# Kernel optimization log

Hardware: AMD Instinct MI355X
Metric: run time of the kernel (lower is better)

## Reference

```python
import jax, jax.numpy as jnp
import numpy as np

WH, WW = 8, 8            # window_size
SH = 2                   # shuffle
NH = 6                   # num_heads
ED = 96                  # embed_dim
NP = WH * WW             # num_patches = 64
S2 = SH * SH             # shuffle group = 4
HD = ED // NH            # head_dim = 16
SCALE = HD ** -0.5 / SH
NW = 2048
NWM = 64
EPS = 1e-5


def _rel_pos_index():
    coords = np.stack(np.meshgrid(np.arange(WH), np.arange(WW), indexing='ij'))  # (2, wh, ww)
    cf = coords.reshape(2, -1)                                # (2, np)
    rel = (cf[:, :, None] - cf[:, None, :]).transpose(1, 2, 0).astype(np.int64)  # (np, np, 2)
    rel[..., 0] += WH - 1
    rel[..., 1] += WW - 1
    rel[..., 0] *= 2 * WW - 1
    return rel.sum(-1).reshape(-1)                            # (np*np,)

_REL_IDX = jnp.asarray(_rel_pos_index())


def setup_inputs() -> dict:
    key = jax.random.key(0)
    ks = jax.random.split(key, 6)
    return {
        'query': jax.random.normal(ks[0], (NW, NP * S2, ED), dtype=jnp.float32),
        'key': jax.random.normal(ks[1], (NW, NP * S2, ED), dtype=jnp.float32),
        'value': jax.random.normal(ks[2], (NW, NP * S2, ED), dtype=jnp.float32),
        'mask': jax.random.normal(ks[3], (NWM, NP, NP), dtype=jnp.float32),
        'bias_table': jax.random.normal(ks[4], (( 2 * WH - 1) * (2 * WW - 1), NH), dtype=jnp.float32) * 0.02,
        'norm_gamma': jnp.ones((S2, ED), dtype=jnp.float32),
        'norm_beta': jnp.zeros((S2, ED), dtype=jnp.float32),
        'proj_w': jax.random.normal(ks[5], (ED, ED), dtype=jnp.float32) * 0.02,
        'proj_b': jnp.zeros((ED,), dtype=jnp.float32),
    }


def reference(query, key, value, mask, bias_table, norm_gamma, norm_beta, proj_w, proj_b):
    nw = query.shape[0]

    def group(x):  # (nw, wh*sh*ww*sw, ed) -> (nw, np, s2, ed)
        x = x.reshape(nw, WH, SH, WW, SH, ED)
        return x.transpose(0, 1, 3, 2, 4, 5).reshape(nw, NP, S2, ED)

    q, k, v = group(query), group(key), group(value)

    # pre-norm LayerNorm over the joint (s2, ed) normalized shape
    mu = q.mean(axis=(-2, -1), keepdims=True)
    var = q.var(axis=(-2, -1), keepdims=True)
    q = (q - mu) / jnp.sqrt(var + EPS) * norm_gamma + norm_beta

    def heads(x):  # (nw, np, s2, ed) -> (nw, nh, np, s2, hd)
        return x.reshape(nw, NP, S2, NH, HD).transpose(0, 3, 1, 2, 4)

    q, k, v = heads(q), heads(k), heads(v)
    q = q * SCALE

    # QK^T contracting jointly over shuffle axis s and head_dim c
    attn = jnp.einsum('wnqsc,wnksc->wnqk', q, k)  # (nw, nh, np, np)

    bias = bias_table[_REL_IDX].reshape(NP, NP, NH).transpose(2, 0, 1)  # (nh, np, np)
    attn = attn + bias[None]

    nwm = mask.shape[0]
    b = nw // nwm
    attn = attn.reshape(b, nwm, NH, NP, NP) + mask[None, :, None]
    attn = jax.nn.softmax(attn.reshape(nw, NH, NP, NP), axis=-1)

    out = jnp.einsum('wnqk,wnksc->wnqsc', attn, v)  # (nw, nh, np, s2, hd)
    out = out.transpose(0, 2, 3, 1, 4).reshape(nw, NP, S2, ED)
    # group_partition_reversed
    out = out.reshape(nw, WH, WW, SH, SH, ED).transpose(0, 1, 3, 2, 4, 5).reshape(nw, NP * S2, ED)
    out = out @ proj_w.T + proj_b
    return out
```

## Files before the change

kernel.cpp:

```cpp
#include <hip/hip_runtime.h>
#include <hip/hip_bf16.h>


#define TPB 256

#define Q0   0
#define K0   8192
#define VT0  16384
#define PR0  24576
#define V_LDS 77824

typedef __attribute__((ext_vector_type(8))) short short8;
typedef __attribute__((ext_vector_type(4))) float f32x4;

union FRAG { uint4 u4; short8 s8; unsigned short us[8]; };

__device__ __forceinline__ int seq_of(int p, int s) {
    return ((p >> 3) << 5) | ((s >> 1) << 4) | ((p & 7) << 1) | (s & 1);
}

#define SWZ(row, slot) (((row) << 7) + ((((slot) ^ ((row) & 7))) << 4))
#define SVK(n) (((n) ^ ((n) >> 3)) & 7)

#define LGKM_FENCE() do { \
    asm volatile("s_waitcnt lgkmcnt(0)" ::: "memory"); \
    __builtin_amdgcn_sched_barrier(0); } while (0)

#define BAR_STAGE() do { \
    asm volatile("s_waitcnt lgkmcnt(0)" ::: "memory"); \
    __builtin_amdgcn_sched_barrier(0); \
    __builtin_amdgcn_s_barrier(); \
    __builtin_amdgcn_sched_barrier(0); } while (0)

#define BAR_WAR() do { \
    __builtin_amdgcn_sched_barrier(0); \
    __builtin_amdgcn_s_barrier(); \
    __builtin_amdgcn_sched_barrier(0); } while (0)

__device__ __forceinline__ unsigned short f2b(float x) {
    union { __hip_bfloat16 h; unsigned short u; } z;
    z.h = __float2bfloat16(x);
    return z.u;
}

__device__ __forceinline__ uint4 pack8(const float* v) {
    union { uint4 u4; unsigned short us[8]; } z;
#pragma unroll
    for (int i = 0; i < 8; ++i) z.us[i] = f2b(v[i]);
    return z.u4;
}

__device__ __forceinline__ void load_pack(const float* src, uint4* dst) {
    float v[16];
#pragma unroll
    for (int i = 0; i < 4; ++i) {
        float4 x = ((const float4*)src)[i];
        v[4 * i] = x.x; v[4 * i + 1] = x.y; v[4 * i + 2] = x.z; v[4 * i + 3] = x.w;
    }
    dst[0] = pack8(v);
    dst[1] = pack8(v + 8);
}

__global__ void build_comb(const float* __restrict__ gmask,
                           const float* __restrict__ gbt,
                           float* __restrict__ comb) {
    const int b = blockIdx.x;
    const int mi = b / 6, n = b - mi * 6;
    const int t = threadIdx.x;
    const float* mrow = gmask + (size_t)mi * 4096;
    float* crow = comb + (size_t)b * 4096;
#pragma unroll
    for (int e = 0; e < 4096; e += TPB) {
        const int i = e + t;
        const int q = i >> 6, k = i & 63;
        const int idx = ((q >> 3) - (k >> 3) + 7) * 15 + ((q & 7) - (k & 7) + 7);
        crow[i] = mrow[i] + gbt[idx * 6 + n];
    }
}

template <int USE_COMB>
__global__ __launch_bounds__(TPB, 2)
void dwa_mfma(const float* __restrict__ gq,
              const float* __restrict__ gk,
              const float* __restrict__ gv,
              const float* __restrict__ gmask,
              const float* __restrict__ gbt,
              const float* __restrict__ ggamma,
              const float* __restrict__ gbeta,
              const float* __restrict__ gpw,
              const float* __restrict__ gpb,
              float* __restrict__ gout,
              const float* __restrict__ comb,
              int nwm)
{
    __shared__ __align__(16) unsigned char Lraw[V_LDS];
    char* L = (char*)Lraw;

    const int w = blockIdx.x;
    const int t = threadIdx.x;
    const int lane = t & 63, wv = t >> 6;
    const int r15 = lane & 15, gsl = lane >> 4;

    const int p_a = t >> 2, s_a = t & 3;
    const int g_a = seq_of(p_a, s_a);
    const size_t rowbase = ((size_t)w * 256 + g_a) * 96;
    const int mbase = (w % nwm) * 4096;
    const int qr0 = (wv << 4) + (gsl << 2);
    const f32x4 zf = {0.f, 0.f, 0.f, 0.f};

    uint4 qreg[12];
    {
        float qv[96];
        float sum = 0.f, ssq = 0.f;
        const float4* qr4 = (const float4*)(gq + rowbase);
#pragma unroll
        for (int i = 0; i < 24; ++i) {
            float4 x = qr4[i];
            qv[4 * i] = x.x; qv[4 * i + 1] = x.y;
            qv[4 * i + 2] = x.z; qv[4 * i + 3] = x.w;
            sum += (x.x + x.y) + (x.z + x.w);
            ssq += (x.x * x.x + x.y * x.y) + (x.z * x.z + x.w * x.w);
        }
        sum += __shfl_xor(sum, 1); ssq += __shfl_xor(ssq, 1);
        sum += __shfl_xor(sum, 2); ssq += __shfl_xor(ssq, 2);
        const float mu = sum * (1.f / 384.f);
        const float rs = rsqrtf(ssq * (1.f / 384.f) - mu * mu + 1e-5f);
        const float4* ga4 = (const float4*)(ggamma + s_a * 96);
        const float4* be4 = (const float4*)(gbeta + s_a * 96);
#pragma unroll
        for (int c6 = 0; c6 < 6; ++c6) {
            float vals[16];
#pragma unroll
            for (int j = 0; j < 4; ++j) {
                float4 g = ga4[c6 * 4 + j];
                float4 b = be4[c6 * 4 + j];
                const int base = c6 * 16 + 4 * j;
                vals[4 * j + 0] = ((qv[base + 0] - mu) * rs * g.x + b.x) * 0.125f;
                vals[4 * j + 1] = ((qv[base + 1] - mu) * rs * g.y + b.y) * 0.125f;
                vals[4 * j + 2] = ((qv[base + 2] - mu) * rs * g.z + b.z) * 0.125f;
                vals[4 * j + 3] = ((qv[base + 3] - mu) * rs * g.w + b.w) * 0.125f;
            }
            qreg[2 * c6]     = pack8(vals);
            qreg[2 * c6 + 1] = pack8(vals + 8);
        }
    }
    uint4 kpf[2][2], vpf[2][2];
    load_pack(gk + rowbase, kpf[0]);
    load_pack(gv + rowbase, vpf[0]);

#pragma unroll
    for (int n = 0; n < 6; ++n) {
        if (n < 5) {
            load_pack(gk + rowbase + (n + 1) * 16, kpf[(n + 1) & 1]);
            load_pack(gv + rowbase + (n + 1) * 16, vpf[(n + 1) & 1]);
        }
        *(uint4*)(L + Q0 + SWZ(p_a, s_a * 2))     = qreg[2 * n];
        *(uint4*)(L + Q0 + SWZ(p_a, s_a * 2 + 1)) = qreg[2 * n + 1];
        *(uint4*)(L + K0 + SWZ(p_a, s_a * 2))     = kpf[n & 1][0];
        *(uint4*)(L + K0 + SWZ(p_a, s_a * 2 + 1)) = kpf[n & 1][1];
#pragma unroll
        for (int h = 0; h < 2; ++h) {
            FRAG u; u.u4 = vpf[n & 1][h];
#pragma unroll
            for (int c = 0; c < 8; ++c) {
                const int np_ = s_a * 16 + h * 8 + c;
                *(unsigned short*)(L + VT0 + (np_ << 7) +
                    (((p_a >> 3) ^ SVK(np_)) << 4) + ((p_a & 7) << 1)) = u.us[c];
            }
        }
        f32x4 sacc[4];
        if (USE_COMB) {
            const float* cb = comb + (size_t)((w % nwm) * 6 + n) * 4096;
#pragma unroll
            for (int tile = 0; tile < 4; ++tile)
#pragma unroll
                for (int r = 0; r < 4; ++r)
                    sacc[tile][r] = cb[((qr0 + r) << 6) + (tile << 4) + r15];
        } else {
#pragma unroll
            for (int tile = 0; tile < 4; ++tile) {
                const int kpx = (tile << 4) + r15;
                const int ik = kpx >> 3, jk = kpx & 7;
#pragma unroll
                for (int r = 0; r < 4; ++r) {
                    const int q = qr0 + r;
                    sacc[tile][r] = gbt[(((q >> 3) - ik + 7) * 15 + ((q & 7) - jk + 7)) * 6 + n]
                                  + gmask[mbase + (q << 6) + kpx];
                }
            }
        }
        BAR_STAGE();

        {
            FRAG a0, a1;
            a0.u4 = *(const uint4*)(L + Q0 + SWZ(wv * 16 + r15, gsl));
            a1.u4 = *(const uint4*)(L + Q0 + SWZ(wv * 16 + r15, 4 + gsl));
#pragma unroll
            for (int tile = 0; tile < 4; ++tile) {
                FRAG b0, b1;
                b0.u4 = *(const uint4*)(L + K0 + SWZ(tile * 16 + r15, gsl));
                b1.u4 = *(const uint4*)(L + K0 + SWZ(tile * 16 + r15, 4 + gsl));
                sacc[tile] = __builtin_amdgcn_mfma_f32_16x16x32_bf16(a0.s8, b0.s8, sacc[tile], 0, 0, 0);
                sacc[tile] = __builtin_amdgcn_mfma_f32_16x16x32_bf16(a1.s8, b1.s8, sacc[tile], 0, 0, 0);
            }
        }

#pragma unroll
        for (int r = 0; r < 4; ++r) {
            const int q = qr0 + r;
            float mx = fmaxf(fmaxf(sacc[0][r], sacc[1][r]),
                             fmaxf(sacc[2][r], sacc[3][r]));
            mx = fmaxf(mx, __shfl_xor(mx, 1));
            mx = fmaxf(mx, __shfl_xor(mx, 2));
            mx = fmaxf(mx, __shfl_xor(mx, 4));
            mx = fmaxf(mx, __shfl_xor(mx, 8));
            float sm = 0.f;
#pragma unroll
            for (int tile = 0; tile < 4; ++tile) {
                sacc[tile][r] = __expf(sacc[tile][r] - mx);
                sm += sacc[tile][r];
            }
            sm += __shfl_xor(sm, 1);
            sm += __shfl_xor(sm, 2);
            sm += __shfl_xor(sm, 4);
            sm += __shfl_xor(sm, 8);
            const float inv = 1.0f / sm;
#pragma unroll
            for (int tile = 0; tile < 4; ++tile) {
                const int col = (tile << 4) + r15;
                *(unsigned short*)(L + Q0 + (q << 7) +
                                   (((col >> 3) ^ (q & 7)) << 4) + ((col & 7) << 1))
                    = f2b(sacc[tile][r] * inv);
            }
        }
        LGKM_FENCE();

        f32x4 oacc[4];
        {
            FRAG pa0, pa1;
            pa0.u4 = *(const uint4*)(L + Q0 + SWZ(wv * 16 + r15, gsl));
            pa1.u4 = *(const uint4*)(L + Q0 + SWZ(wv * 16 + r15, 4 + gsl));
#pragma unroll
            for (int ct = 0; ct < 4; ++ct) {
                const int nr = ct * 16 + r15;
                const int sv = SVK(nr);
                FRAG b0, b1;
                b0.u4 = *(const uint4*)(L + VT0 + (nr << 7) + ((gsl ^ sv) << 4));
                b1.u4 = *(const uint4*)(L + VT0 + (nr << 7) + (((4 + gsl) ^ sv) << 4));
                oacc[ct] = __builtin_amdgcn_mfma_f32_16x16x32_bf16(pa0.s8, b0.s8, zf, 0, 0, 0);
                oacc[ct] = __builtin_amdgcn_mfma_f32_16x16x32_bf16(pa1.s8, b1.s8, oacc[ct], 0, 0, 0);
            }
        }

#pragma unroll
        for (int ct = 0; ct < 4; ++ct)
#pragma unroll
            for (int r = 0; r < 4; ++r) {
                const int token = ((qr0 + r) << 2) + ct;
                *(unsigned short*)(L + PR0 + token * 208 + ((n << 4) + r15) * 2)
                    = f2b(oacc[ct][r]);
            }
        if (n < 5) BAR_WAR();
    }

    LGKM_FENCE();
    {
        FRAG bw[3][6];
#pragma unroll
        for (int kk = 0; kk < 3; ++kk)
#pragma unroll
            for (int ct = 0; ct < 6; ++ct) {
                const int o = (ct << 4) + r15;
                const float4* wp = (const float4*)(gpw + o * 96 + kk * 32 + (gsl << 3));
                float4 w0 = wp[0], w1 = wp[1];
                float w8[8] = {w0.x, w0.y, w0.z, w0.w, w1.x, w1.y, w1.z, w1.w};
                bw[kk][ct].u4 = pack8(w8);
            }
        float pbv[6];
#pragma unroll
        for (int ct = 0; ct < 6; ++ct) pbv[ct] = gpb[(ct << 4) + r15];

#pragma unroll
        for (int mt = 0; mt < 4; ++mt) {
            const int rowA = (wv << 6) + (mt << 4) + r15;
            FRAG A[3];
#pragma unroll
            for (int kk = 0; kk < 3; ++kk)
                A[kk].u4 = *(const uint4*)(L + PR0 + rowA * 208 + kk * 64 + (gsl << 4));
            f32x4 acc[6];
#pragma unroll
            for (int ct = 0; ct < 6; ++ct) {
                acc[ct] = __builtin_amdgcn_mfma_f32_16x16x32_bf16(A[0].s8, bw[0][ct].s8, zf, 0, 0, 0);
                acc[ct] = __builtin_amdgcn_mfma_f32_16x16x32_bf16(A[1].s8, bw[1][ct].s8, acc[ct], 0, 0, 0);
                acc[ct] = __builtin_amdgcn_mfma_f32_16x16x32_bf16(A[2].s8, bw[2][ct].s8, acc[ct], 0, 0, 0);
            }
#pragma unroll
            for (int ct = 0; ct < 6; ++ct)
#pragma unroll
                for (int rr = 0; rr < 4; ++rr) {
                    const int token = (wv << 6) + (mt << 4) + (gsl << 2) + rr;
                    const int p = token >> 2, s = token & 3;
                    const int gsq = seq_of(p, s);
                    gout[((size_t)w * 256 + gsq) * 96 + (ct << 4) + r15]
                        = acc[ct][rr] + pbv[ct];
                }
        }
    }
}

extern "C" void kernel_launch(void* const* d_in, const int* in_sizes, int n_in,
                              void* d_out, int out_size, void* d_ws, size_t ws_size,
                              hipStream_t stream) {
    const float* gq     = (const float*)d_in[0];
    const float* gk     = (const float*)d_in[1];
    const float* gv     = (const float*)d_in[2];
    const float* gmask  = (const float*)d_in[3];
    const float* gbt    = (const float*)d_in[4];
    const float* ggamma = (const float*)d_in[5];
    const float* gbeta  = (const float*)d_in[6];
    const float* gpw    = (const float*)d_in[7];
    const float* gpb    = (const float*)d_in[8];
    float* gout = (float*)d_out;

    const int nw  = in_sizes[0] / (256 * 96);
    const int nwm = in_sizes[3] / (64 * 64);
    const size_t comb_bytes = (size_t)nwm * 6 * 4096 * sizeof(float);

    if (ws_size >= comb_bytes) {
        float* comb = (float*)d_ws;
        build_comb<<<nwm * 6, TPB, 0, stream>>>(gmask, gbt, comb);
        dwa_mfma<1><<<nw, TPB, 0, stream>>>(gq, gk, gv, gmask, gbt, ggamma, gbeta,
                                            gpw, gpb, gout, comb, nwm);
    } else {
        dwa_mfma<0><<<nw, TPB, 0, stream>>>(gq, gk, gv, gmask, gbt, ggamma, gbeta,
                                            gpw, gpb, gout, (const float*)nullptr, nwm);
    }
}
```

Baseline: 279.9 us.

## Stream Q per head with double-buffered raw prefetch instead of holding packed Q

Instead of keeping the whole normalized Q row packed in registers, the kernel now computes only the LayerNorm statistics up front and re-reads Q per head. Raw Q/K/V and the bias/mask tile for the next head are prefetched into a ping-pong register set, and gamma/beta are staged in LDS. The head loop is manually unrolled by two and no longer fully unrolled. The aim is lower register pressure and better overlap of global loads with compute, at the cost of reading Q twice and using a little more LDS.

```diff
diff --git a/kernel.cpp b/kernel.cpp
--- a/kernel.cpp
+++ b/kernel.cpp
@@ -8,7 +8,9 @@
 #define K0   8192
 #define VT0  16384
 #define PR0  24576
-#define V_LDS 77824
+#define GA0  77824
+#define BE0  79360
+#define V_LDS 80896
 
 typedef __attribute__((ext_vector_type(8))) short short8;
 typedef __attribute__((ext_vector_type(4))) float f32x4;
@@ -48,17 +50,6 @@
 #pragma unroll
     for (int i = 0; i < 8; ++i) z.us[i] = f2b(v[i]);
     return z.u4;
-}
-
-__device__ __forceinline__ void load_pack(const float* src, uint4* dst) {
-    float v[16];
-#pragma unroll
-    for (int i = 0; i < 4; ++i) {
-        float4 x = ((const float4*)src)[i];
-        v[4 * i] = x.x; v[4 * i + 1] = x.y; v[4 * i + 2] = x.z; v[4 * i + 3] = x.w;
-    }
-    dst[0] = pack8(v);
-    dst[1] = pack8(v + 8);
 }
 
 __global__ void build_comb(const float* __restrict__ gmask,
@@ -77,6 +68,133 @@
         crow[i] = mrow[i] + gbt[idx * 6 + n];
     }
 }
+
+#define PREFETCH(NN, QQ, KK, VV, SS)                                           \
+    {                                                                          \
+        if (USE_COMB) {                                                        \
+            const float* cb = comb + (size_t)((w % nwm) * 6 + (NN)) * 4096;    \
+            _Pragma("unroll")                                                  \
+            for (int tile = 0; tile < 4; ++tile)                               \
+                _Pragma("unroll")                                              \
+                for (int r = 0; r < 4; ++r)                                    \
+                    SS[tile][r] = cb[((qr0 + r) << 6) + (tile << 4) + r15];    \
+        } else {                                                               \
+            _Pragma("unroll")                                                  \
+            for (int tile = 0; tile < 4; ++tile) {                             \
+                const int kpx = (tile << 4) + r15;                             \
+                const int ik = kpx >> 3, jk = kpx & 7;                         \
+                _Pragma("unroll")                                              \
+                for (int r = 0; r < 4; ++r) {                                  \
+                    const int q = qr0 + r;                                     \
+                    SS[tile][r] = gbt[(((q >> 3) - ik + 7) * 15 +              \
+                                      ((q & 7) - jk + 7)) * 6 + (NN)]          \
+                                + gmask[mbase + (q << 6) + kpx];               \
+                }                                                              \
+            }                                                                  \
+        }                                                                      \
+        const float4* qp_ = (const float4*)(gq + rowbase + (NN) * 16);         \
+        const float4* kp_ = (const float4*)(gk + rowbase + (NN) * 16);         \
+        const float4* vp_ = (const float4*)(gv + rowbase + (NN) * 16);         \
+        _Pragma("unroll")                                                      \
+        for (int i = 0; i < 4; ++i) {                                          \
+            QQ[i] = qp_[i]; KK[i] = kp_[i]; VV[i] = vp_[i];                    \
+        }                                                                      \
+    }
+
+#define STAGE_QKV(NN, QQ, KK, VV)                                              \
+    {                                                                          \
+        const float* ga_ = s_ga + s_a * 96 + (NN) * 16;                        \
+        const float* be_ = s_be + s_a * 96 + (NN) * 16;                        \
+        float xq[16], xk[16], xv[16];                                          \
+        _Pragma("unroll")                                                      \
+        for (int i = 0; i < 4; ++i) {                                          \
+            xq[4*i+0]=QQ[i].x; xq[4*i+1]=QQ[i].y; xq[4*i+2]=QQ[i].z; xq[4*i+3]=QQ[i].w; \
+            xk[4*i+0]=KK[i].x; xk[4*i+1]=KK[i].y; xk[4*i+2]=KK[i].z; xk[4*i+3]=KK[i].w; \
+            xv[4*i+0]=VV[i].x; xv[4*i+1]=VV[i].y; xv[4*i+2]=VV[i].z; xv[4*i+3]=VV[i].w; \
+        }                                                                      \
+        _Pragma("unroll")                                                      \
+        for (int i = 0; i < 16; ++i)                                           \
+            xq[i] = ((xq[i] - mu) * rs * ga_[i] + be_[i]) * 0.125f;            \
+        *(uint4*)(L + Q0 + SWZ(p_a, s_a * 2))     = pack8(xq);                 \
+        *(uint4*)(L + Q0 + SWZ(p_a, s_a * 2 + 1)) = pack8(xq + 8);             \
+        *(uint4*)(L + K0 + SWZ(p_a, s_a * 2))     = pack8(xk);                 \
+        *(uint4*)(L + K0 + SWZ(p_a, s_a * 2 + 1)) = pack8(xk + 8);             \
+        _Pragma("unroll")                                                      \
+        for (int c = 0; c < 16; ++c) {                                         \
+            const int np_ = s_a * 16 + c;                                      \
+            *(unsigned short*)(L + VT0 + (np_ << 7) +                          \
+                (((p_a >> 3) ^ SVK(np_)) << 4) + ((p_a & 7) << 1)) = f2b(xv[c]); \
+        }                                                                      \
+    }
+
+#define COMPUTE_HEAD(NN, SS)                                                   \
+    {                                                                          \
+        {                                                                      \
+            FRAG a0, a1;                                                       \
+            a0.u4 = *(const uint4*)(L + Q0 + SWZ(wv * 16 + r15, gsl));         \
+            a1.u4 = *(const uint4*)(L + Q0 + SWZ(wv * 16 + r15, 4 + gsl));     \
+            _Pragma("unroll")                                                  \
+            for (int tile = 0; tile < 4; ++tile) {                             \
+                FRAG b0, b1;                                                   \
+                b0.u4 = *(const uint4*)(L + K0 + SWZ(tile * 16 + r15, gsl));   \
+                b1.u4 = *(const uint4*)(L + K0 + SWZ(tile * 16 + r15, 4 + gsl)); \
+                SS[tile] = __builtin_amdgcn_mfma_f32_16x16x32_bf16(a0.s8, b0.s8, SS[tile], 0, 0, 0); \
+                SS[tile] = __builtin_amdgcn_mfma_f32_16x16x32_bf16(a1.s8, b1.s8, SS[tile], 0, 0, 0); \
+            }                                                                  \
+        }                                                                      \
+        _Pragma("unroll")                                                      \
+        for (int r = 0; r < 4; ++r) {                                          \
+            const int q = qr0 + r;                                             \
+            float mx = fmaxf(fmaxf(SS[0][r], SS[1][r]), fmaxf(SS[2][r], SS[3][r])); \
+            mx = fmaxf(mx, __shfl_xor(mx, 1));                                 \
+            mx = fmaxf(mx, __shfl_xor(mx, 2));                                 \
+            mx = fmaxf(mx, __shfl_xor(mx, 4));                                 \
+            mx = fmaxf(mx, __shfl_xor(mx, 8));                                 \
+            float sm = 0.f;                                                    \
+            _Pragma("unroll")                                                  \
+            for (int tile = 0; tile < 4; ++tile) {                             \
+                SS[tile][r] = __expf(SS[tile][r] - mx);                        \
+                sm += SS[tile][r];                                             \
+            }                                                                  \
+            sm += __shfl_xor(sm, 1);                                           \
+            sm += __shfl_xor(sm, 2);                                           \
+            sm += __shfl_xor(sm, 4);                                           \
+            sm += __shfl_xor(sm, 8);                                           \
+            const float inv = 1.0f / sm;                                       \
+            _Pragma("unroll")                                                  \
+            for (int tile = 0; tile < 4; ++tile) {                             \
+                const int col = (tile << 4) + r15;                             \
+                *(unsigned short*)(L + Q0 + (q << 7) +                         \
+                    (((col >> 3) ^ (q & 7)) << 4) + ((col & 7) << 1))          \
+                    = f2b(SS[tile][r] * inv);                                  \
+            }                                                                  \
+        }                                                                      \
+        LGKM_FENCE();                                                          \
+        f32x4 oacc[4];                                                         \
+        {                                                                      \
+            FRAG pa0, pa1;                                                     \
+            pa0.u4 = *(const uint4*)(L + Q0 + SWZ(wv * 16 + r15, gsl));        \
+            pa1.u4 = *(const uint4*)(L + Q0 + SWZ(wv * 16 + r15, 4 + gsl));    \
+            _Pragma("unroll")                                                  \
+            for (int ct = 0; ct < 4; ++ct) {                                   \
+                const int nr = ct * 16 + r15;                                  \
+                const int sv = SVK(nr);                                        \
+                FRAG b0, b1;                                                   \
+                b0.u4 = *(const uint4*)(L + VT0 + (nr << 7) + ((gsl ^ sv) << 4)); \
+                b1.u4 = *(const uint4*)(L + VT0 + (nr << 7) + (((4 + gsl) ^ sv) << 4)); \
+                oacc[ct] = __builtin_amdgcn_mfma_f32_16x16x32_bf16(pa0.s8, b0.s8, zf, 0, 0, 0); \
+                oacc[ct] = __builtin_amdgcn_mfma_f32_16x16x32_bf16(pa1.s8, b1.s8, oacc[ct], 0, 0, 0); \
+            }                                                                  \
+        }                                                                      \
+        _Pragma("unroll")                                                      \
+        for (int ct = 0; ct < 4; ++ct)                                         \
+            _Pragma("unroll")                                                  \
+            for (int r = 0; r < 4; ++r) {                                      \
+                const int token = ((qr0 + r) << 2) + ct;                       \
+                *(unsigned short*)(L + PR0 + token * 208 + (((NN) << 4) + r15) * 2) \
+                    = f2b(oacc[ct][r]);                                        \
+            }                                                                  \
+    }
 
 template <int USE_COMB>
 __global__ __launch_bounds__(TPB, 2)
@@ -108,159 +226,48 @@
     const int qr0 = (wv << 4) + (gsl << 2);
     const f32x4 zf = {0.f, 0.f, 0.f, 0.f};
 
-    uint4 qreg[12];
+    float* s_ga = (float*)(L + GA0);
+    float* s_be = (float*)(L + BE0);
+
+    float mu, rs;
     {
-        float qv[96];
+        const float4* qr4 = (const float4*)(gq + rowbase);
         float sum = 0.f, ssq = 0.f;
-        const float4* qr4 = (const float4*)(gq + rowbase);
 #pragma unroll
         for (int i = 0; i < 24; ++i) {
             float4 x = qr4[i];
-            qv[4 * i] = x.x; qv[4 * i + 1] = x.y;
-            qv[4 * i + 2] = x.z; qv[4 * i + 3] = x.w;
             sum += (x.x + x.y) + (x.z + x.w);
             ssq += (x.x * x.x + x.y * x.y) + (x.z * x.z + x.w * x.w);
         }
         sum += __shfl_xor(sum, 1); ssq += __shfl_xor(ssq, 1);
         sum += __shfl_xor(sum, 2); ssq += __shfl_xor(ssq, 2);
-        const float mu = sum * (1.f / 384.f);
-        const float rs = rsqrtf(ssq * (1.f / 384.f) - mu * mu + 1e-5f);
-        const float4* ga4 = (const float4*)(ggamma + s_a * 96);
-        const float4* be4 = (const float4*)(gbeta + s_a * 96);
-#pragma unroll
-        for (int c6 = 0; c6 < 6; ++c6) {
-            float vals[16];
-#pragma unroll
-            for (int j = 0; j < 4; ++j) {
-                float4 g = ga4[c6 * 4 + j];
-                float4 b = be4[c6 * 4 + j];
-                const int base = c6 * 16 + 4 * j;
-                vals[4 * j + 0] = ((qv[base + 0] - mu) * rs * g.x + b.x) * 0.125f;
-                vals[4 * j + 1] = ((qv[base + 1] - mu) * rs * g.y + b.y) * 0.125f;
-                vals[4 * j + 2] = ((qv[base + 2] - mu) * rs * g.z + b.z) * 0.125f;
-                vals[4 * j + 3] = ((qv[base + 3] - mu) * rs * g.w + b.w) * 0.125f;
-            }
-            qreg[2 * c6]     = pack8(vals);
-            qreg[2 * c6 + 1] = pack8(vals + 8);
-        }
-    }
-    uint4 kpf[2][2], vpf[2][2];
-    load_pack(gk + rowbase, kpf[0]);
-    load_pack(gv + rowbase, vpf[0]);
-
-#pragma unroll
-    for (int n = 0; n < 6; ++n) {
-        if (n < 5) {
-            load_pack(gk + rowbase + (n + 1) * 16, kpf[(n + 1) & 1]);
-            load_pack(gv + rowbase + (n + 1) * 16, vpf[(n + 1) & 1]);
-        }
-        *(uint4*)(L + Q0 + SWZ(p_a, s_a * 2))     = qreg[2 * n];
-        *(uint4*)(L + Q0 + SWZ(p_a, s_a * 2 + 1)) = qreg[2 * n + 1];
-        *(uint4*)(L + K0 + SWZ(p_a, s_a * 2))     = kpf[n & 1][0];
-        *(uint4*)(L + K0 + SWZ(p_a, s_a * 2 + 1)) = kpf[n & 1][1];
-#pragma unroll
-        for (int h = 0; h < 2; ++h) {
-            FRAG u; u.u4 = vpf[n & 1][h];
-#pragma unroll
-            for (int c = 0; c < 8; ++c) {
-                const int np_ = s_a * 16 + h * 8 + c;
-                *(unsigned short*)(L + VT0 + (np_ << 7) +
-                    (((p_a >> 3) ^ SVK(np_)) << 4) + ((p_a & 7) << 1)) = u.us[c];
-            }
-        }
-        f32x4 sacc[4];
-        if (USE_COMB) {
-            const float* cb = comb + (size_t)((w % nwm) * 6 + n) * 4096;
-#pragma unroll
-            for (int tile = 0; tile < 4; ++tile)
-#pragma unroll
-                for (int r = 0; r < 4; ++r)
-                    sacc[tile][r] = cb[((qr0 + r) << 6) + (tile << 4) + r15];
-        } else {
-#pragma unroll
-            for (int tile = 0; tile < 4; ++tile) {
-                const int kpx = (tile << 4) + r15;
-                const int ik = kpx >> 3, jk = kpx & 7;
-#pragma unroll
-                for (int r = 0; r < 4; ++r) {
-                    const int q = qr0 + r;
-                    sacc[tile][r] = gbt[(((q >> 3) - ik + 7) * 15 + ((q & 7) - jk + 7)) * 6 + n]
-                                  + gmask[mbase + (q << 6) + kpx];
-                }
-            }
-        }
+        mu = sum * (1.f / 384.f);
+        rs = rsqrtf(ssq * (1.f / 384.f) - mu * mu + 1e-5f);
+    }
+    for (int i = t; i < 384; i += TPB) {
+        s_ga[i] = ggamma[i];
+        s_be[i] = gbeta[i];
+    }
+
+    float4 qA[4], kA[4], vA[4], qB[4], kB[4], vB[4];
+    f32x4 sA[4], sB[4];
+
+    PREFETCH(0, qA, kA, vA, sA);
+    BAR_STAGE();
+
+#pragma unroll 1
+    for (int nh = 0; nh < 3; ++nh) {
+        const int n0 = nh * 2;
+        STAGE_QKV(n0, qA, kA, vA);
+        PREFETCH(n0 + 1, qB, kB, vB, sB);
         BAR_STAGE();
-
-        {
-            FRAG a0, a1;
-            a0.u4 = *(const uint4*)(L + Q0 + SWZ(wv * 16 + r15, gsl));
-            a1.u4 = *(const uint4*)(L + Q0 + SWZ(wv * 16 + r15, 4 + gsl));
-#pragma unroll
-            for (int tile = 0; tile < 4; ++tile) {
-                FRAG b0, b1;
-                b0.u4 = *(const uint4*)(L + K0 + SWZ(tile * 16 + r15, gsl));
-                b1.u4 = *(const uint4*)(L + K0 + SWZ(tile * 16 + r15, 4 + gsl));
-                sacc[tile] = __builtin_amdgcn_mfma_f32_16x16x32_bf16(a0.s8, b0.s8, sacc[tile], 0, 0, 0);
-                sacc[tile] = __builtin_amdgcn_mfma_f32_16x16x32_bf16(a1.s8, b1.s8, sacc[tile], 0, 0, 0);
-            }
-        }
-
-#pragma unroll
-        for (int r = 0; r < 4; ++r) {
-            const int q = qr0 + r;
-            float mx = fmaxf(fmaxf(sacc[0][r], sacc[1][r]),
-                             fmaxf(sacc[2][r], sacc[3][r]));
-            mx = fmaxf(mx, __shfl_xor(mx, 1));
-            mx = fmaxf(mx, __shfl_xor(mx, 2));
-            mx = fmaxf(mx, __shfl_xor(mx, 4));
-            mx = fmaxf(mx, __shfl_xor(mx, 8));
-            float sm = 0.f;
-#pragma unroll
-            for (int tile = 0; tile < 4; ++tile) {
-                sacc[tile][r] = __expf(sacc[tile][r] - mx);
-                sm += sacc[tile][r];
-            }
-            sm += __shfl_xor(sm, 1);
-            sm += __shfl_xor(sm, 2);
-            sm += __shfl_xor(sm, 4);
-            sm += __shfl_xor(sm, 8);
-            const float inv = 1.0f / sm;
-#pragma unroll
-            for (int tile = 0; tile < 4; ++tile) {
-                const int col = (tile << 4) + r15;
-                *(unsigned short*)(L + Q0 + (q << 7) +
-                                   (((col >> 3) ^ (q & 7)) << 4) + ((col & 7) << 1))
-                    = f2b(sacc[tile][r] * inv);
-            }
-        }
-        LGKM_FENCE();
-
-        f32x4 oacc[4];
-        {
-            FRAG pa0, pa1;
-            pa0.u4 = *(const uint4*)(L + Q0 + SWZ(wv * 16 + r15, gsl));
-            pa1.u4 = *(const uint4*)(L + Q0 + SWZ(wv * 16 + r15, 4 + gsl));
-#pragma unroll
-            for (int ct = 0; ct < 4; ++ct) {
-                const int nr = ct * 16 + r15;
-                const int sv = SVK(nr);
-                FRAG b0, b1;
-                b0.u4 = *(const uint4*)(L + VT0 + (nr << 7) + ((gsl ^ sv) << 4));
-                b1.u4 = *(const uint4*)(L + VT0 + (nr << 7) + (((4 + gsl) ^ sv) << 4));
-                oacc[ct] = __builtin_amdgcn_mfma_f32_16x16x32_bf16(pa0.s8, b0.s8, zf, 0, 0, 0);
-                oacc[ct] = __builtin_amdgcn_mfma_f32_16x16x32_bf16(pa1.s8, b1.s8, oacc[ct], 0, 0, 0);
-            }
-        }
-
-#pragma unroll
-        for (int ct = 0; ct < 4; ++ct)
-#pragma unroll
-            for (int r = 0; r < 4; ++r) {
-                const int token = ((qr0 + r) << 2) + ct;
-                *(unsigned short*)(L + PR0 + token * 208 + ((n << 4) + r15) * 2)
-                    = f2b(oacc[ct][r]);
-            }
-        if (n < 5) BAR_WAR();
+        COMPUTE_HEAD(n0, sA);
+        BAR_WAR();
+        STAGE_QKV(n0 + 1, qB, kB, vB);
+        if (nh < 2) PREFETCH(n0 + 2, qA, kA, vA, sA);
+        BAR_STAGE();
+        COMPUTE_HEAD(n0 + 1, sB);
+        if (nh < 2) BAR_WAR();
     }
 
     LGKM_FENCE();
```

New measurement: 269.7 us. 3.6% less time.
